# Optimization experiments

Measured on AMD Instinct MI355X. Metric: run time of the kernel, lower is better.

## Reference

```python
import jax, jax.numpy as jnp
import numpy as np

EMB = 768
N_HEADS = 12
HEAD_DIM = EMB // N_HEADS
EPS = 1e-5


def _gelu_tanh(x):
    c = jnp.sqrt(jnp.asarray(2.0 / jnp.pi, x.dtype))
    return 0.5 * x * (1.0 + jnp.tanh(c * (x + 0.044715 * x ** 3)))


def _layernorm(x, scale, shift):
    mean = jnp.mean(x, axis=-1, keepdims=True)
    var = jnp.mean((x - mean) ** 2, axis=-1, keepdims=True)
    return (x - mean) / jnp.sqrt(var + EPS) * scale + shift


def setup_inputs() -> dict:
    key = jax.random.key(0)
    ks = jax.random.split(key, 8)
    s = 0.02  # GPT-2 style init scale
    x = jax.random.normal(ks[0], (8, 1024, EMB), dtype=jnp.float32)
    # torch Linear weights are (out, in); no biases (qkv_bias=False everywhere)
    wq = jax.random.normal(ks[1], (EMB, EMB), dtype=jnp.float32) * s
    wk = jax.random.normal(ks[2], (EMB, EMB), dtype=jnp.float32) * s
    wv = jax.random.normal(ks[3], (EMB, EMB), dtype=jnp.float32) * s
    wo = jax.random.normal(ks[4], (EMB, EMB), dtype=jnp.float32) * s
    w1 = jax.random.normal(ks[5], (4 * EMB, EMB), dtype=jnp.float32) * s
    w2 = jax.random.normal(ks[6], (EMB, 4 * EMB), dtype=jnp.float32) * s
    ln1_scale = jnp.ones((EMB,), jnp.float32)
    ln1_shift = jnp.zeros((EMB,), jnp.float32)
    ln2_scale = jnp.ones((EMB,), jnp.float32)
    ln2_shift = jnp.zeros((EMB,), jnp.float32)
    return dict(x=x, wq=wq, wk=wk, wv=wv, wo=wo, w1=w1, w2=w2,
                ln1_scale=ln1_scale, ln1_shift=ln1_shift,
                ln2_scale=ln2_scale, ln2_shift=ln2_shift)


def reference(x, wq, wk, wv, wo, w1, w2, ln1_scale, ln1_shift, ln2_scale, ln2_shift):
    B, T, E = x.shape
    # --- attention sublayer (pre-LN) ---
    h = _layernorm(x, ln1_scale, ln1_shift)
    q = (h @ wq.T).reshape(B, T, N_HEADS, HEAD_DIM).transpose(0, 2, 1, 3)
    k = (h @ wk.T).reshape(B, T, N_HEADS, HEAD_DIM).transpose(0, 2, 1, 3)
    v = (h @ wv.T).reshape(B, T, N_HEADS, HEAD_DIM).transpose(0, 2, 1, 3)
    scores = jnp.einsum('bhqd,bhkd->bhqk', q, k)  # [B,H,T,T]
    causal = jnp.tril(jnp.ones((T, T), dtype=bool))
    scores = jnp.where(causal, scores, -jnp.inf)
    attn = jax.nn.softmax(scores / np.sqrt(HEAD_DIM), axis=-1)
    ctx = jnp.einsum('bhqk,bhkd->bhqd', attn, v)
    ctx = ctx.transpose(0, 2, 1, 3).reshape(B, T, E)
    x = x + ctx @ wo.T
    # --- FFN sublayer (pre-LN) ---
    h = _layernorm(x, ln2_scale, ln2_shift)
    h = _gelu_tanh(h @ w1.T) @ w2.T
    return x + h
```

## Files before the change

### kernel.cpp

```cpp
#include <hip/hip_runtime.h>
#include <hip/hip_bf16.h>
#include <cstdint>

#define EMB    768
#define NHEADS 12
#define HDIM   64
#define SEQ    1024
#define BATCH  8
#define MROWS  (BATCH*SEQ)
#define FFN    3072
#define W2E    (EMB*EMB)
#define W4E    (FFN*EMB)

typedef __bf16 bf16_t;
typedef bf16_t bf16x8 __attribute__((ext_vector_type(8)));
typedef float  f32x4  __attribute__((ext_vector_type(4)));

__device__ __forceinline__ float b2f(unsigned short u) {
    union { unsigned int i; float f; } t; t.i = ((unsigned int)u) << 16; return t.f;
}
__device__ __forceinline__ unsigned short f2b(float f) {
    union { float f; unsigned int i; } t; t.f = f;
    unsigned int lsb = (t.i >> 16) & 1u;
    t.i += 0x7fffu + lsb;
    return (unsigned short)(t.i >> 16);
}
__device__ __forceinline__ float fexp2(float x) {
#if defined(__has_builtin)
#if __has_builtin(__builtin_amdgcn_exp2f)
    return __builtin_amdgcn_exp2f(x);
#else
    return exp2f(x);
#endif
#else
    return exp2f(x);
#endif
}
__device__ __forceinline__ float frcp(float x) {
#if defined(__has_builtin)
#if __has_builtin(__builtin_amdgcn_rcpf)
    return __builtin_amdgcn_rcpf(x);
#else
    return 1.f / x;
#endif
#else
    return 1.f / x;
#endif
}
__device__ __forceinline__ float gelu_f(float x) {
    float x2 = x * x;
    float u  = x * __builtin_fmaf(x2, -0.10294823f, -2.3022082f);
    return x * frcp(1.f + fexp2(u));
}

#if defined(__has_builtin)
#if __has_builtin(__builtin_amdgcn_global_load_lds)
#define HAS_GLL 1
#endif
#endif
#ifndef HAS_GLL
#define HAS_GLL 0
#endif

__device__ __forceinline__ void gll16(const unsigned short* g, unsigned short* lds_wave_base) {
#if HAS_GLL
    __builtin_amdgcn_global_load_lds(
        (const __attribute__((address_space(1))) unsigned int*)g,
        (__attribute__((address_space(3))) unsigned int*)lds_wave_base, 16, 0, 0);
#endif
}
__device__ __forceinline__ void stage16(const unsigned short* g, unsigned short* lds_wave_base, int lane) {
#if HAS_GLL
    __builtin_amdgcn_global_load_lds(
        (const __attribute__((address_space(1))) unsigned int*)g,
        (__attribute__((address_space(3))) unsigned int*)lds_wave_base, 16, 0, 0);
#else
    *reinterpret_cast<int4*>(lds_wave_base + lane * 8) = *reinterpret_cast<const int4*>(g);
#endif
}

__device__ __forceinline__ int4 load8(const void* src, size_t eoff, bool f32) {
    if (f32) {
        const float4* p = reinterpret_cast<const float4*>((const float*)src + eoff);
        float4 a = p[0], b = p[1];
        union { unsigned short u[8]; int4 v; } r;
        r.u[0] = f2b(a.x); r.u[1] = f2b(a.y); r.u[2] = f2b(a.z); r.u[3] = f2b(a.w);
        r.u[4] = f2b(b.x); r.u[5] = f2b(b.y); r.u[6] = f2b(b.z); r.u[7] = f2b(b.w);
        return r.v;
    }
    return *reinterpret_cast<const int4*>((const unsigned short*)src + eoff);
}
__device__ __forceinline__ float4 load4f(const void* src, size_t eoff, bool f32) {
    if (f32) return *reinterpret_cast<const float4*>((const float*)src + eoff);
    ushort4 u = *reinterpret_cast<const ushort4*>((const unsigned short*)src + eoff);
    float4 r; r.x = b2f(u.x); r.y = b2f(u.y); r.z = b2f(u.z); r.w = b2f(u.w);
    return r;
}

struct DetectArgs { const unsigned short* p[11]; int n[11]; };

__global__ __launch_bounds__(256) void detect_all(DetectArgs a, int* __restrict__ flags) {
    __shared__ int cnt;
    if (threadIdx.x == 0) cnt = 0;
    __syncthreads();
    const unsigned short* src = a.p[blockIdx.x];
    int npairs = a.n[blockIdx.x] / 2;
    if (npairs > 4096) npairs = 4096;
    int local = 0;
    for (int p = threadIdx.x; p < npairs; p += 256) {
        unsigned short u0 = src[2 * p], u1 = src[2 * p + 1];
        int e0 = (u0 >> 7) & 0xFF;
        bool insane0 = (e0 == 0xFF) || (u0 != 0 && (e0 < 96 || e0 > 159));
        bool zpat    = (u0 == 0 && u1 != 0);
        if (insane0 || zpat) ++local;
    }
    atomicAdd(&cnt, local);
    __syncthreads();
    if (threadIdx.x == 0) flags[blockIdx.x] = (cnt * 8 > npairs) ? 1 : 0;
}

__global__ __launch_bounds__(256) void cvt_adapt(
        const void* __restrict__ src, unsigned short* __restrict__ dst,
        int n, const int* __restrict__ flag) {
    int i = blockIdx.x * 256 + threadIdx.x;
    if (i * 4 >= n) return;
    if (*flag) {
        float4 f = reinterpret_cast<const float4*>(src)[i];
        ushort4 o;
        o.x = f2b(f.x); o.y = f2b(f.y); o.z = f2b(f.z); o.w = f2b(f.w);
        reinterpret_cast<ushort4*>(dst)[i] = o;
    } else {
        reinterpret_cast<ushort4*>(dst)[i] = reinterpret_cast<const ushort4*>(src)[i];
    }
}

struct CvtArgs {
    const void* src[6];
    unsigned short* dst[6];
    int n[6];
    int blkoff[7];
    const int* F;
    int fidx[6];
};
__global__ __launch_bounds__(256) void cvt_weights(CvtArgs a) {
    int b = blockIdx.x, seg = 0;
    #pragma unroll
    for (int s = 0; s < 6; ++s) if (b >= a.blkoff[s + 1]) seg = s + 1;
    int i = (b - a.blkoff[seg]) * 256 + threadIdx.x;
    if (i * 4 >= a.n[seg]) return;
    if (a.F[a.fidx[seg]]) {
        float4 f = reinterpret_cast<const float4*>(a.src[seg])[i];
        ushort4 o;
        o.x = f2b(f.x); o.y = f2b(f.y); o.z = f2b(f.z); o.w = f2b(f.w);
        reinterpret_cast<ushort4*>(a.dst[seg])[i] = o;
    } else {
        reinterpret_cast<ushort4*>(a.dst[seg])[i] =
            reinterpret_cast<const ushort4*>(a.src[seg])[i];
    }
}

__global__ __launch_bounds__(256) void reduce2_kernel(
        const float* __restrict__ P, const unsigned short* __restrict__ resid,
        float* __restrict__ out, int n4) {
    int i = blockIdx.x * 256 + threadIdx.x;
    if (i >= n4) return;
    float4 a = reinterpret_cast<const float4*>(P)[i];
    float4 b = reinterpret_cast<const float4*>(P + (size_t)MROWS * EMB)[i];
    ushort4 r = reinterpret_cast<const ushort4*>(resid)[i];
    float4 o;
    o.x = a.x + b.x + b2f(r.x);
    o.y = a.y + b.y + b2f(r.y);
    o.z = a.z + b.z + b2f(r.z);
    o.w = a.w + b.w + b2f(r.w);
    reinterpret_cast<float4*>(out)[i] = o;
}

__global__ __launch_bounds__(256) void ln_kernel(
        const void* __restrict__ x,     const int* __restrict__ fx,
        const void* __restrict__ scale, const int* __restrict__ fsc,
        const void* __restrict__ shift, const int* __restrict__ fsh,
        unsigned short* __restrict__ out) {
    const bool xf = fx && *fx, scf = fsc && *fsc, shf = fsh && *fsh;
    int wave = threadIdx.x >> 6;
    int lane = threadIdx.x & 63;
    int row  = blockIdx.x * 4 + wave;
    const size_t rbase = (size_t)row * EMB;
    float v[12];
    float s = 0.f, s2 = 0.f;
    #pragma unroll
    for (int i = 0; i < 3; ++i) {
        float4 a = load4f(x, rbase + i * 256 + lane * 4, xf);
        v[i*4+0] = a.x; v[i*4+1] = a.y; v[i*4+2] = a.z; v[i*4+3] = a.w;
        s  += a.x + a.y + a.z + a.w;
        s2 += a.x*a.x + a.y*a.y + a.z*a.z + a.w*a.w;
    }
    #pragma unroll
    for (int off = 1; off < 64; off <<= 1) {
        s  += __shfl_xor(s,  off);
        s2 += __shfl_xor(s2, off);
    }
    float mean = s * (1.f / EMB);
    float var  = fmaxf(s2 * (1.f / EMB) - mean * mean, 0.f);
    float rstd = rsqrtf(var + 1e-5f);
    unsigned short* orow = out + rbase;
    #pragma unroll
    for (int i = 0; i < 3; ++i) {
        float4 sc = load4f(scale, i * 256 + lane * 4, scf);
        float4 sh = load4f(shift, i * 256 + lane * 4, shf);
        ushort4 o;
        o.x = f2b((v[i*4+0] - mean) * rstd * sc.x + sh.x);
        o.y = f2b((v[i*4+1] - mean) * rstd * sc.y + sh.y);
        o.z = f2b((v[i*4+2] - mean) * rstd * sc.z + sh.z);
        o.w = f2b((v[i*4+3] - mean) * rstd * sc.w + sh.w);
        *reinterpret_cast<ushort4*>(orow + i * 256 + lane * 4) = o;
    }
}

template<bool GELU, bool RESID, bool OUTF32>
__global__ __launch_bounds__(256, 3) void gemm_lds(
        const unsigned short* __restrict__ A,
        const unsigned short* __restrict__ W,
        const void* R, const int* __restrict__ fR, size_t rOff,
        void* C, int M, int N, int K, int lda, int ldw) {
    constexpr int BK = 32;
    __shared__ __align__(16) unsigned short sA[2][128 * BK];
    __shared__ __align__(16) unsigned short sB[2][128 * BK];
    const int m0 = blockIdx.x * 128, n0 = blockIdx.y * 128;
    const int kz = blockIdx.z;
    const int t = threadIdx.x, wave = t >> 6;
    const int lane = t & 63;
    const int wrow = (wave >> 1) * 64, wcol = (wave & 1) * 64;
    const int quad = lane >> 4, lr = lane & 15;
    const int r0 = t >> 2;
    const int scg = (t & 3) ^ ((t >> 3) & 3);
    const int c0 = scg * 8;
    const int xq = quad ^ ((lr >> 1) & 3);
    const bool rf = fR && *fR;

    A += (size_t)kz * K;
    W += (size_t)kz * K;

    f32x4 acc[4][4];
    #pragma unroll
    for (int i = 0; i < 4; ++i)
        #pragma unroll
        for (int j = 0; j < 4; ++j)
            acc[i][j] = (f32x4){0.f, 0.f, 0.f, 0.f};

    const unsigned short* gA0 = A + (size_t)(m0 + r0) * lda + c0;
    const unsigned short* gA1 = A + (size_t)(m0 + 64 + r0) * lda + c0;
    const unsigned short* gB0 = W + (size_t)(n0 + r0) * ldw + c0;
    const unsigned short* gB1 = W + (size_t)(n0 + 64 + r0) * ldw + c0;

#if HAS_GLL
    gll16(gA0, sA[0] + wave * 512);
    gll16(gA1, sA[0] + 2048 + wave * 512);
    gll16(gB0, sB[0] + wave * 512);
    gll16(gB1, sB[0] + 2048 + wave * 512);
#else
    *reinterpret_cast<int4*>(sA[0] + t * 8)        = *reinterpret_cast<const int4*>(gA0);
    *reinterpret_cast<int4*>(sA[0] + 2048 + t * 8) = *reinterpret_cast<const int4*>(gA1);
    *reinterpret_cast<int4*>(sB[0] + t * 8)        = *reinterpret_cast<const int4*>(gB0);
    *reinterpret_cast<int4*>(sB[0] + 2048 + t * 8) = *reinterpret_cast<const int4*>(gB1);
#endif
    __syncthreads();

    int buf = 0;
    for (int k0 = 0; k0 < K; k0 += BK) {
        if (k0 + BK < K) {
            const int pf = buf ^ 1;
            const int kn = k0 + BK;
#if HAS_GLL
            gll16(gA0 + kn, sA[pf] + wave * 512);
            gll16(gA1 + kn, sA[pf] + 2048 + wave * 512);
            gll16(gB0 + kn, sB[pf] + wave * 512);
            gll16(gB1 + kn, sB[pf] + 2048 + wave * 512);
#else
            *reinterpret_cast<int4*>(sA[pf] + t * 8)        = *reinterpret_cast<const int4*>(gA0 + kn);
            *reinterpret_cast<int4*>(sA[pf] + 2048 + t * 8) = *reinterpret_cast<const int4*>(gA1 + kn);
            *reinterpret_cast<int4*>(sB[pf] + t * 8)        = *reinterpret_cast<const int4*>(gB0 + kn);
            *reinterpret_cast<int4*>(sB[pf] + 2048 + t * 8) = *reinterpret_cast<const int4*>(gB1 + kn);
#endif
        }
        bf16x8 af[4], bfv[4];
        #pragma unroll
        for (int i = 0; i < 4; ++i)
            af[i] = *reinterpret_cast<const bf16x8*>(
                sA[buf] + (wrow >> 6) * 2048 + (i * 16 + lr) * 32 + xq * 8);
        #pragma unroll
        for (int j = 0; j < 4; ++j)
            bfv[j] = *reinterpret_cast<const bf16x8*>(
                sB[buf] + (wcol >> 6) * 2048 + (j * 16 + lr) * 32 + xq * 8);
        #pragma unroll
        for (int i = 0; i < 4; ++i)
            #pragma unroll
            for (int j = 0; j < 4; ++j)
                acc[i][j] = __builtin_amdgcn_mfma_f32_16x16x32_bf16(af[i], bfv[j], acc[i][j], 0, 0, 0);
        __syncthreads();
        buf ^= 1;
    }

    float* Cf = (float*)C + (size_t)kz * M * N;
    #pragma unroll
    for (int i = 0; i < 4; ++i) {
        #pragma unroll
        for (int j = 0; j < 4; ++j) {
            #pragma unroll
            for (int r = 0; r < 4; ++r) {
                int row = m0 + wrow + i * 16 + quad * 4 + r;
                int col = n0 + wcol + j * 16 + lr;
                float val = acc[i][j][r];
                if (GELU) val = gelu_f(val);
                size_t idx = (size_t)row * N + col;
                if (RESID) {
                    float rv = rf ? ((const float*)R)[idx + rOff]
                                  : b2f(((const unsigned short*)R)[idx + rOff]);
                    val += rv;
                }
                if (OUTF32) Cf[idx] = val;
                else {
                    bf16_t hv = (bf16_t)val;
                    ((unsigned short*)C)[idx] = *reinterpret_cast<unsigned short*>(&hv);
                }
            }
        }
    }
}

template<bool GELU, bool RESID, bool OUTF32>
__global__ __launch_bounds__(256) void gemm_bt(
        const unsigned short* __restrict__ A,
        const void* __restrict__ W, const int* __restrict__ fW,
        const void* R, const int* __restrict__ fR, size_t rOff,
        void* C,
        int M, int N, int K) {
    const bool wf = fW && *fW;
    const bool rf = fR && *fR;
    constexpr int BK = 32, PAD = 8, LDW = BK + PAD;
    __shared__ __align__(16) unsigned short sA[128 * LDW];
    __shared__ __align__(16) unsigned short sB[128 * LDW];
    const int m0 = blockIdx.x * 128;
    const int n0 = blockIdx.y * 128;
    const int t    = threadIdx.x;
    const int wave = t >> 6, lane = t & 63;
    const int wrow = (wave >> 1) * 64, wcol = (wave & 1) * 64;
    const int quad = lane >> 4, lr = lane & 15;
    const int srow = t >> 2, scol = (t & 3) * 8;

    f32x4 acc[4][4];
    #pragma unroll
    for (int i = 0; i < 4; ++i)
        #pragma unroll
        for (int j = 0; j < 4; ++j)
            acc[i][j] = (f32x4){0.f, 0.f, 0.f, 0.f};

    const size_t aBase = (size_t)(m0 + srow) * K + scol;
    const size_t bBase = (size_t)(n0 + srow) * K + scol;

    for (int k0 = 0; k0 < K; k0 += BK) {
        int4 av0 = *reinterpret_cast<const int4*>(A + aBase + k0);
        int4 av1 = *reinterpret_cast<const int4*>(A + aBase + (size_t)64 * K + k0);
        int4 bv0 = load8(W, bBase + k0, wf);
        int4 bv1 = load8(W, bBase + (size_t)64 * K + k0, wf);
        *reinterpret_cast<int4*>(sA + srow * LDW + scol)        = av0;
        *reinterpret_cast<int4*>(sA + (srow + 64) * LDW + scol) = av1;
        *reinterpret_cast<int4*>(sB + srow * LDW + scol)        = bv0;
        *reinterpret_cast<int4*>(sB + (srow + 64) * LDW + scol) = bv1;
        __syncthreads();
        bf16x8 af[4], bfv[4];
        #pragma unroll
        for (int i = 0; i < 4; ++i)
            af[i] = *reinterpret_cast<const bf16x8*>(sA + (wrow + i * 16 + lr) * LDW + quad * 8);
        #pragma unroll
        for (int j = 0; j < 4; ++j)
            bfv[j] = *reinterpret_cast<const bf16x8*>(sB + (wcol + j * 16 + lr) * LDW + quad * 8);
        #pragma unroll
        for (int i = 0; i < 4; ++i)
            #pragma unroll
            for (int j = 0; j < 4; ++j)
                acc[i][j] = __builtin_amdgcn_mfma_f32_16x16x32_bf16(af[i], bfv[j], acc[i][j], 0, 0, 0);
        __syncthreads();
    }

    #pragma unroll
    for (int i = 0; i < 4; ++i) {
        #pragma unroll
        for (int j = 0; j < 4; ++j) {
            #pragma unroll
            for (int r = 0; r < 4; ++r) {
                int row = m0 + wrow + i * 16 + quad * 4 + r;
                int col = n0 + wcol + j * 16 + lr;
                float val = acc[i][j][r];
                if (GELU) val = gelu_f(val);
                size_t idx = (size_t)row * N + col;
                if (RESID) {
                    float rv = rf ? ((const float*)R)[idx + rOff]
                                  : b2f(((const unsigned short*)R)[idx + rOff]);
                    val += rv;
                }
                if (OUTF32) ((float*)C)[idx] = val;
                else        ((unsigned short*)C)[idx] = f2b(val);
            }
        }
    }
}

__global__ __launch_bounds__(256) void fattn_kernel(
        const unsigned short* __restrict__ q,
        const unsigned short* __restrict__ k,
        const unsigned short* __restrict__ v,
        int rs, unsigned short* __restrict__ ctx) {
    constexpr int VTP = 72;
    __shared__ __align__(16) unsigned short sK[2][64 * 64];
    __shared__ __align__(16) unsigned short Vt[2][64 * VTP];
    __shared__ __align__(16) unsigned short Pl[4][16 * VTP];
    const int tid  = threadIdx.x;
    const int wave = tid >> 6, lane = tid & 63;
    const int quad = lane >> 4, lr = lane & 15;
    const int NH   = gridDim.x >> 3;
    const int head = blockIdx.x % NH;
    const int pr   = blockIdx.x / NH;
    const int bb   = head / NHEADS, hd = head % NHEADS;
    const size_t seqbase = (size_t)bb * SEQ;
    constexpr float C2 = 0.18033688011112042f;

    const int krow0 = tid >> 3;
    const int dreal = ((tid & 7) * 8) ^ ((krow0 & 7) << 3);
    const int vrow = tid >> 2;
    const int vcol = (tid & 3) * 16;
    const int vxr  = vrow ^ ((tid & 3) << 4);
    const int kswz = (lr & 7) << 3;
    const int pswr = ((lr >> 2) & 3) << 3;
    unsigned short* Pw = Pl[wave];

    #pragma unroll
    for (int seg = 0; seg < 2; ++seg) {
        const int qt = seg == 0 ? (15 - pr) : pr;
        const int q0 = qt * 64 + wave * 16;

        bf16x8 aQ0, aQ1;
        {
            const unsigned short* qp = q + (seqbase + q0 + lr) * rs + hd * HDIM + quad * 8;
            aQ0 = *reinterpret_cast<const bf16x8*>(qp);
            aQ1 = *reinterpret_cast<const bf16x8*>(qp + 32);
        }

        f32x4 O[4];
        #pragma unroll
        for (int i = 0; i < 4; ++i) O[i] = (f32x4){0.f, 0.f, 0.f, 0.f};
        float mrow[4], lrow[4];
        #pragma unroll
        for (int r = 0; r < 4; ++r) { mrow[r] = -__builtin_inff(); lrow[r] = 0.f; }

        {
            const unsigned short* kp = k + (seqbase + krow0) * rs + hd * HDIM + dreal;
            stage16(kp,                   &sK[0][wave * 512],        lane);
            stage16(kp + (size_t)32 * rs, &sK[0][2048 + wave * 512], lane);
            const unsigned short* vp = v + (seqbase + vrow) * rs + hd * HDIM + vcol;
            union { int4 v4; unsigned short u[8]; } pa, pb;
            pa.v4 = *reinterpret_cast<const int4*>(vp);
            pb.v4 = *reinterpret_cast<const int4*>(vp + 8);
            #pragma unroll
            for (int e = 0; e < 8; ++e) Vt[0][(vcol + e) * VTP + vxr]     = pa.u[e];
            #pragma unroll
            for (int e = 0; e < 8; ++e) Vt[0][(vcol + 8 + e) * VTP + vxr] = pb.u[e];
        }
        __syncthreads();

        for (int kt = 0; kt <= qt; ++kt) {
            const int b = kt & 1;
            union { int4 v4; unsigned short u[8]; } ua, ub;
            if (kt < qt) {
                const unsigned short* kp = k + (seqbase + (size_t)(kt + 1) * 64 + krow0) * rs
                                         + hd * HDIM + dreal;
                stage16(kp,                   &sK[b ^ 1][wave * 512],        lane);
                stage16(kp + (size_t)32 * rs, &sK[b ^ 1][2048 + wave * 512], lane);
                const unsigned short* vp = v + (seqbase + (size_t)(kt + 1) * 64 + vrow) * rs
                                         + hd * HDIM + vcol;
                ua.v4 = *reinterpret_cast<const int4*>(vp);
                ub.v4 = *reinterpret_cast<const int4*>(vp + 8);
            }

            f32x4 S[4];
            #pragma unroll
            for (int sub = 0; sub < 4; ++sub) {
                const unsigned short* kr = &sK[b][(sub * 16 + lr) * 64];
                bf16x8 b0 = *reinterpret_cast<const bf16x8*>(kr + ((quad * 8) ^ kswz));
                bf16x8 b1 = *reinterpret_cast<const bf16x8*>(kr + ((32 + quad * 8) ^ kswz));
                f32x4 accS = (f32x4){0.f, 0.f, 0.f, 0.f};
                accS = __builtin_amdgcn_mfma_f32_16x16x32_bf16(aQ0, b0, accS, 0, 0, 0);
                accS = __builtin_amdgcn_mfma_f32_16x16x32_bf16(aQ1, b1, accS, 0, 0, 0);
                S[sub] = accS;
            }
            const bool diag = (kt == qt);
            #pragma unroll
            for (int sub = 0; sub < 4; ++sub) {
                const int kg = kt * 64 + sub * 16 + lr;
                #pragma unroll
                for (int r = 0; r < 4; ++r) {
                    float s = S[sub][r] * C2;
                    if (diag && kg > q0 + quad * 4 + r) s = -__builtin_inff();
                    S[sub][r] = s;
                }
            }
            float mnew[4], alpha[4];
            #pragma unroll
            for (int r = 0; r < 4; ++r) {
                float mx = fmaxf(fmaxf(S[0][r], S[1][r]), fmaxf(S[2][r], S[3][r]));
                #pragma unroll
                for (int m = 1; m < 16; m <<= 1) mx = fmaxf(mx, __shfl_xor(mx, m));
                mnew[r]  = fmaxf(mrow[r], mx);
                alpha[r] = fexp2(mrow[r] - mnew[r]);
                mrow[r]  = mnew[r];
            }
            float rsum[4] = {0.f, 0.f, 0.f, 0.f};
            #pragma unroll
            for (int sub = 0; sub < 4; ++sub)
                #pragma unroll
                for (int r = 0; r < 4; ++r) {
                    float p = fexp2(S[sub][r] - mnew[r]);
                    S[sub][r] = p;
                    rsum[r] += p;
                }
            #pragma unroll
            for (int r = 0; r < 4; ++r) {
                float rs2 = rsum[r];
                #pragma unroll
                for (int m = 1; m < 16; m <<= 1) rs2 += __shfl_xor(rs2, m);
                lrow[r] = lrow[r] * alpha[r] + rs2;
            }

            #pragma unroll
            for (int sub = 0; sub < 4; ++sub)
                #pragma unroll
                for (int r = 0; r < 4; ++r) {
                    bf16_t hv = (bf16_t)S[sub][r];
                    Pw[(quad * 4 + r) * VTP + ((sub * 16 + lr) ^ (quad << 3))] =
                        *reinterpret_cast<unsigned short*>(&hv);
                }
            if (kt < qt) {
                #pragma unroll
                for (int e = 0; e < 8; ++e) Vt[b ^ 1][(vcol + e) * VTP + vxr]     = ua.u[e];
                #pragma unroll
                for (int e = 0; e < 8; ++e) Vt[b ^ 1][(vcol + 8 + e) * VTP + vxr] = ub.u[e];
            }
            #pragma unroll
            for (int d = 0; d < 4; ++d)
                #pragma unroll
                for (int r = 0; r < 4; ++r)
                    O[d][r] *= alpha[r];

            #pragma unroll
            for (int c = 0; c < 2; ++c) {
                bf16x8 aP = *reinterpret_cast<const bf16x8*>(
                    &Pw[lr * VTP + ((c * 32 + quad * 8) ^ pswr)]);
                #pragma unroll
                for (int d = 0; d < 4; ++d) {
                    bf16x8 bV = *reinterpret_cast<const bf16x8*>(
                        &Vt[b][(d * 16 + lr) * VTP + ((c * 32 + quad * 8) ^ (d << 4))]);
                    O[d] = __builtin_amdgcn_mfma_f32_16x16x32_bf16(aP, bV, O[d], 0, 0, 0);
                }
            }
            __syncthreads();
        }

        #pragma unroll
        for (int r = 0; r < 4; ++r) {
            const float rinv = 1.f / lrow[r];
            const int qg = q0 + quad * 4 + r;
            unsigned short* crow = ctx + (seqbase + qg) * EMB + hd * HDIM;
            #pragma unroll
            for (int d = 0; d < 4; ++d)
                crow[d * 16 + lr] = f2b(O[d][r] * rinv);
        }
    }
}

extern "C" void kernel_launch(void* const* d_in, const int* in_sizes, int n_in,
                              void* d_out, int out_size, void* d_ws, size_t ws_size,
                              hipStream_t stream) {
    const void* x  = d_in[0];
    const void* wq = d_in[1], *wk = d_in[2], *wv = d_in[3], *wo = d_in[4];
    const void* w1 = d_in[5], *w2 = d_in[6];
    const void* g1 = d_in[7], *s1 = d_in[8], *g2 = d_in[9], *s2 = d_in[10];
    char* ws = (char*)d_ws;
    dim3 blk(256);

    int* F = (int*)ws;
    {
        DetectArgs da;
        for (int i = 0; i < 11; ++i) { da.p[i] = (const unsigned short*)d_in[i]; da.n[i] = in_sizes[i]; }
        detect_all<<<11, blk, 0, stream>>>(da, F);
    }

    const size_t SZE = (size_t)MROWS * EMB;
    const size_t SZB = SZE * 2;
    unsigned short* base = (unsigned short*)(ws + 256);
    dim3 g768(MROWS / 128, EMB / 128);

    const size_t FULLB = 256 + 2ULL * (2 * W4E) + 2ULL * (4 * W2E)
                       + 2ULL * ((size_t)MROWS * 2304) + 2 * SZB
                       + 2ULL * ((size_t)MROWS * FFN);
    const size_t FULLB2 = FULLB + 2ULL * SZE * 4;

    if (ws_size >= FULLB2) {
        unsigned short* w1b   = base;
        unsigned short* w2b   = w1b + W4E;
        unsigned short* wqkvb = w2b + W4E;
        unsigned short* wob   = wqkvb + 3 * W2E;
        unsigned short* P     = wob + W2E;
        unsigned short* B0    = P + (size_t)MROWS * 2304;
        unsigned short* B1    = B0 + SZE;
        unsigned short* G     = B1 + SZE;
        float*          PK    = (float*)(G + (size_t)MROWS * FFN);

        {
            CvtArgs ca;
            ca.src[0] = wq; ca.src[1] = wk; ca.src[2] = wv;
            ca.src[3] = wo; ca.src[4] = w1; ca.src[5] = w2;
            ca.dst[0] = wqkvb; ca.dst[1] = wqkvb + W2E; ca.dst[2] = wqkvb + 2 * W2E;
            ca.dst[3] = wob;   ca.dst[4] = w1b;         ca.dst[5] = w2b;
            ca.n[0] = ca.n[1] = ca.n[2] = ca.n[3] = W2E; ca.n[4] = ca.n[5] = W4E;
            int off = 0;
            for (int s = 0; s < 6; ++s) { ca.blkoff[s] = off; off += ca.n[s] / 1024; }
            ca.blkoff[6] = off;
            ca.F = F;
            ca.fidx[0] = 1; ca.fidx[1] = 2; ca.fidx[2] = 3;
            ca.fidx[3] = 4; ca.fidx[4] = 5; ca.fidx[5] = 6;
            cvt_weights<<<off, blk, 0, stream>>>(ca);
        }

        ln_kernel<<<MROWS / 4, blk, 0, stream>>>(x, F+0, g1, F+7, s1, F+8, B1);
        dim3 gqkv(MROWS / 128, 2304 / 128);
        gemm_lds<false, false, false><<<gqkv, blk, 0, stream>>>(B1, wqkvb, nullptr, nullptr, 0, P, MROWS, 2304, EMB, EMB, EMB);
        fattn_kernel<<<BATCH * NHEADS * 8, blk, 0, stream>>>(P, P + 768, P + 1536, 2304, B0);
        gemm_lds<false, true, false><<<g768, blk, 0, stream>>>(B0, wob, x, F+0, 0, B1, MROWS, EMB, EMB, EMB, EMB);
        ln_kernel<<<MROWS / 4, blk, 0, stream>>>(B1, nullptr, g2, F+9, s2, F+10, B0);
        dim3 gffn1(MROWS / 128, FFN / 128);
        gemm_lds<true, false, false><<<gffn1, blk, 0, stream>>>(B0, w1b, nullptr, nullptr, 0, G, MROWS, FFN, EMB, EMB, EMB);
        dim3 gsk(MROWS / 128, EMB / 128, 2);
        gemm_lds<false, false, true><<<gsk, blk, 0, stream>>>(G, w2b, nullptr, nullptr, 0, PK, MROWS, EMB, FFN / 2, FFN, FFN);
        reduce2_kernel<<<(SZE / 4 + 255) / 256, blk, 0, stream>>>(PK, B1, (float*)d_out, SZE / 4);
    } else if (ws_size >= FULLB) {
        unsigned short* w1b   = base;
        unsigned short* w2b   = w1b + W4E;
        unsigned short* wqkvb = w2b + W4E;
        unsigned short* wob   = wqkvb + 3 * W2E;
        unsigned short* P     = wob + W2E;
        unsigned short* B0    = P + (size_t)MROWS * 2304;
        unsigned short* B1    = B0 + SZE;
        unsigned short* G     = B1 + SZE;

        {
            CvtArgs ca;
            ca.src[0] = wq; ca.src[1] = wk; ca.src[2] = wv;
            ca.src[3] = wo; ca.src[4] = w1; ca.src[5] = w2;
            ca.dst[0] = wqkvb; ca.dst[1] = wqkvb + W2E; ca.dst[2] = wqkvb + 2 * W2E;
            ca.dst[3] = wob;   ca.dst[4] = w1b;         ca.dst[5] = w2b;
            ca.n[0] = ca.n[1] = ca.n[2] = ca.n[3] = W2E; ca.n[4] = ca.n[5] = W4E;
            int off = 0;
            for (int s = 0; s < 6; ++s) { ca.blkoff[s] = off; off += ca.n[s] / 1024; }
            ca.blkoff[6] = off;
            ca.F = F;
            ca.fidx[0] = 1; ca.fidx[1] = 2; ca.fidx[2] = 3;
            ca.fidx[3] = 4; ca.fidx[4] = 5; ca.fidx[5] = 6;
            cvt_weights<<<off, blk, 0, stream>>>(ca);
        }

        ln_kernel<<<MROWS / 4, blk, 0, stream>>>(x, F+0, g1, F+7, s1, F+8, B1);
        dim3 gqkv(MROWS / 128, 2304 / 128);
        gemm_lds<false, false, false><<<gqkv, blk, 0, stream>>>(B1, wqkvb, nullptr, nullptr, 0, P, MROWS, 2304, EMB, EMB, EMB);
        fattn_kernel<<<BATCH * NHEADS * 8, blk, 0, stream>>>(P, P + 768, P + 1536, 2304, B0);
        gemm_lds<false, true, false><<<g768, blk, 0, stream>>>(B0, wob, x, F+0, 0, B1, MROWS, EMB, EMB, EMB, EMB);
        ln_kernel<<<MROWS / 4, blk, 0, stream>>>(B1, nullptr, g2, F+9, s2, F+10, B0);
        dim3 gffn1(MROWS / 128, FFN / 128);
        gemm_lds<true, false, false><<<gffn1, blk, 0, stream>>>(B0, w1b, nullptr, nullptr, 0, G, MROWS, FFN, EMB, EMB, EMB);
        gemm_lds<false, true, true><<<g768, blk, 0, stream>>>(G, w2b, B1, nullptr, 0, d_out, MROWS, EMB, FFN, FFN, FFN);
    } else if (ws_size >= 256 + 4 * SZB) {
        unsigned short* B0 = base;
        unsigned short* B1 = B0 + SZE;
        unsigned short* B2 = B1 + SZE;
        unsigned short* B3 = B2 + SZE;
        ln_kernel<<<MROWS / 4, blk, 0, stream>>>(x, F+0, g1, F+7, s1, F+8, B0);
        gemm_bt<false, false, false><<<g768, blk, 0, stream>>>(B0, wq, F+1, nullptr, nullptr, 0, B1, MROWS, EMB, EMB);
        gemm_bt<false, false, false><<<g768, blk, 0, stream>>>(B0, wk, F+2, nullptr, nullptr, 0, B2, MROWS, EMB, EMB);
        gemm_bt<false, false, false><<<g768, blk, 0, stream>>>(B0, wv, F+3, nullptr, nullptr, 0, B3, MROWS, EMB, EMB);
        fattn_kernel<<<BATCH * NHEADS * 8, blk, 0, stream>>>(B1, B2, B3, EMB, B0);
        gemm_bt<false, true, false><<<g768, blk, 0, stream>>>(B0, wo, F+4, x, F+0, 0, B1, MROWS, EMB, EMB);
        ln_kernel<<<MROWS / 4, blk, 0, stream>>>(B1, nullptr, g2, F+9, s2, F+10, B2);
        dim3 c3072(2048 / 128, FFN / 128), c768(2048 / 128, EMB / 128);
        for (int c = 0; c < 4; ++c) {
            const size_t r0 = (size_t)c * 2048;
            gemm_bt<true, false, false><<<c3072, blk, 0, stream>>>(B2 + r0 * EMB, w1, F+5, nullptr, nullptr, 0, B3, 2048, FFN, EMB);
            gemm_bt<false, true, true><<<c768, blk, 0, stream>>>(B3, w2, F+6, B1 + r0 * EMB, nullptr, 0, (float*)d_out + r0 * EMB, 2048, EMB, FFN);
        }
    } else {
        unsigned short* hlow = (unsigned short*)d_out;
        unsigned short* x2up = (unsigned short*)d_out + SZE;
        unsigned short* wsQ = base;
        unsigned short* wsK = wsQ + (size_t)1024 * EMB;
        unsigned short* wsV = wsK + (size_t)1024 * EMB;
        unsigned short* wsC = wsV + (size_t)1024 * EMB;
        ln_kernel<<<MROWS / 4, blk, 0, stream>>>(x, F+0, g1, F+7, s1, F+8, hlow);
        dim3 q768(1024 / 128, EMB / 128);
        for (int grp = 0; grp < BATCH; ++grp) {
            const size_t r0 = (size_t)grp * 1024;
            gemm_bt<false, false, false><<<q768, blk, 0, stream>>>(hlow + r0 * EMB, wq, F+1, nullptr, nullptr, 0, wsQ, 1024, EMB, EMB);
            gemm_bt<false, false, false><<<q768, blk, 0, stream>>>(hlow + r0 * EMB, wk, F+2, nullptr, nullptr, 0, wsK, 1024, EMB, EMB);
            gemm_bt<false, false, false><<<q768, blk, 0, stream>>>(hlow + r0 * EMB, wv, F+3, nullptr, nullptr, 0, wsV, 1024, EMB, EMB);
            fattn_kernel<<<1 * NHEADS * 8, blk, 0, stream>>>(wsQ, wsK, wsV, EMB, wsC);
            gemm_bt<false, true, false><<<q768, blk, 0, stream>>>(wsC, wo, F+4, x, F+0, r0 * EMB, x2up + r0 * EMB, 1024, EMB, EMB);
        }
        unsigned short* xb = base;
        unsigned short* h2 = xb + (size_t)1024 * EMB;
        unsigned short* gb = h2 + (size_t)1024 * EMB;
        dim3 f3072(1024 / 128, FFN / 128), f768(1024 / 128, EMB / 128);
        for (int c = 0; c < BATCH; ++c) {
            const size_t r0 = (size_t)c * 1024;
            hipMemcpyAsync(xb, x2up + r0 * EMB, (size_t)1024 * EMB * 2,
                           hipMemcpyDeviceToDevice, stream);
            ln_kernel<<<1024 / 4, blk, 0, stream>>>(xb, nullptr, g2, F+9, s2, F+10, h2);
            gemm_bt<true, false, false><<<f3072, blk, 0, stream>>>(h2, w1, F+5, nullptr, nullptr, 0, gb, 1024, FFN, EMB);
            gemm_bt<false, true, true><<<f768, blk, 0, stream>>>(gb, w2, F+6, xb, nullptr, 0, (float*)d_out + r0 * EMB, 1024, EMB, FFN);
        }
    }
}
```

Baseline: 390.6 us.

## Triple-buffer GEMM LDS tiles with explicit vmcnt waits and raw barriers

Moves the bf16 GEMM main loop from double-buffered to triple-buffered LDS staging on the global-load-to-LDS path, so prefetches run two K-tiles ahead. It uses explicit s_waitcnt vmcnt counts and a raw s_barrier instead of __syncthreads, so the wait only covers the tile about to be consumed. This aims to hide global load latency better. LDS use per block rises from 32KB to 48KB, which may lower occupancy below the 3 blocks/CU launch bound, and the hand-written waitcnt logic is fragile.

Result: faster. 379.1 us (-2.9%).

```diff
diff --git a/kernel.cpp b/kernel.cpp
--- a/kernel.cpp
+++ b/kernel.cpp
@@ -223,8 +223,8 @@
         const void* R, const int* __restrict__ fR, size_t rOff,
         void* C, int M, int N, int K, int lda, int ldw) {
     constexpr int BK = 32;
-    __shared__ __align__(16) unsigned short sA[2][128 * BK];
-    __shared__ __align__(16) unsigned short sB[2][128 * BK];
+    __shared__ __align__(16) unsigned short sA[3][128 * BK];
+    __shared__ __align__(16) unsigned short sB[3][128 * BK];
     const int m0 = blockIdx.x * 128, n0 = blockIdx.y * 128;
     const int kz = blockIdx.z;
     const int t = threadIdx.x, wave = t >> 6;
@@ -252,53 +252,96 @@
     const unsigned short* gB0 = W + (size_t)(n0 + r0) * ldw + c0;
     const unsigned short* gB1 = W + (size_t)(n0 + 64 + r0) * ldw + c0;
 
+    const int nk = K / BK;
+
 #if HAS_GLL
-    gll16(gA0, sA[0] + wave * 512);
-    gll16(gA1, sA[0] + 2048 + wave * 512);
-    gll16(gB0, sB[0] + wave * 512);
-    gll16(gB1, sB[0] + 2048 + wave * 512);
+    #define STAGE_T(tile, bsel)                                       \
+        do {                                                          \
+            const int kk_ = (tile) * BK;                              \
+            gll16(gA0 + kk_, sA[bsel] + wave * 512);                  \
+            gll16(gA1 + kk_, sA[bsel] + 2048 + wave * 512);           \
+            gll16(gB0 + kk_, sB[bsel] + wave * 512);                  \
+            gll16(gB1 + kk_, sB[bsel] + 2048 + wave * 512);           \
+        } while (0)
+
+    STAGE_T(0, 0);
+    if (nk > 1) {
+        STAGE_T(1, 1);
+        asm volatile("s_waitcnt vmcnt(4)" ::: "memory");
+    } else {
+        asm volatile("s_waitcnt vmcnt(0)" ::: "memory");
+    }
+    __builtin_amdgcn_s_barrier();
+    asm volatile("" ::: "memory");
+
+    int cur = 0;
+    for (int i = 0; i < nk; ++i) {
+        if (i + 2 < nk) {
+            int pf = cur + 2; if (pf >= 3) pf -= 3;
+            STAGE_T(i + 2, pf);
+        }
+        bf16x8 af[4], bfv[4];
+        #pragma unroll
+        for (int ii = 0; ii < 4; ++ii)
+            af[ii] = *reinterpret_cast<const bf16x8*>(
+                sA[cur] + (wrow >> 6) * 2048 + (ii * 16 + lr) * 32 + xq * 8);
+        #pragma unroll
+        for (int j = 0; j < 4; ++j)
+            bfv[j] = *reinterpret_cast<const bf16x8*>(
+                sB[cur] + (wcol >> 6) * 2048 + (j * 16 + lr) * 32 + xq * 8);
+        #pragma unroll
+        for (int ii = 0; ii < 4; ++ii)
+            #pragma unroll
+            for (int j = 0; j < 4; ++j)
+                acc[ii][j] = __builtin_amdgcn_mfma_f32_16x16x32_bf16(af[ii], bfv[j], acc[ii][j], 0, 0, 0);
+        if (i + 2 < nk) {
+            asm volatile("s_waitcnt vmcnt(4)" ::: "memory");
+        } else if (i + 1 < nk) {
+            asm volatile("s_waitcnt vmcnt(0)" ::: "memory");
+        }
+        if (i + 1 < nk) {
+            __builtin_amdgcn_s_barrier();
+            asm volatile("" ::: "memory");
+        }
+        cur += 1; if (cur == 3) cur = 0;
+    }
+    #undef STAGE_T
 #else
-    *reinterpret_cast<int4*>(sA[0] + t * 8)        = *reinterpret_cast<const int4*>(gA0);
-    *reinterpret_cast<int4*>(sA[0] + 2048 + t * 8) = *reinterpret_cast<const int4*>(gA1);
-    *reinterpret_cast<int4*>(sB[0] + t * 8)        = *reinterpret_cast<const int4*>(gB0);
-    *reinterpret_cast<int4*>(sB[0] + 2048 + t * 8) = *reinterpret_cast<const int4*>(gB1);
-#endif
-    __syncthreads();
-
-    int buf = 0;
-    for (int k0 = 0; k0 < K; k0 += BK) {
-        if (k0 + BK < K) {
-            const int pf = buf ^ 1;
-            const int kn = k0 + BK;
-#if HAS_GLL
-            gll16(gA0 + kn, sA[pf] + wave * 512);
-            gll16(gA1 + kn, sA[pf] + 2048 + wave * 512);
-            gll16(gB0 + kn, sB[pf] + wave * 512);
-            gll16(gB1 + kn, sB[pf] + 2048 + wave * 512);
-#else
+    int cur = 0;
+    {
+        *reinterpret_cast<int4*>(sA[0] + t * 8)        = *reinterpret_cast<const int4*>(gA0);
+        *reinterpret_cast<int4*>(sA[0] + 2048 + t * 8) = *reinterpret_cast<const int4*>(gA1);
+        *reinterpret_cast<int4*>(sB[0] + t * 8)        = *reinterpret_cast<const int4*>(gB0);
+        *reinterpret_cast<int4*>(sB[0] + 2048 + t * 8) = *reinterpret_cast<const int4*>(gB1);
+        __syncthreads();
+    }
+    for (int i = 0; i < nk; ++i) {
+        if (i + 1 < nk) {
+            int pf = cur ^ 1;
+            const int kn = (i + 1) * BK;
             *reinterpret_cast<int4*>(sA[pf] + t * 8)        = *reinterpret_cast<const int4*>(gA0 + kn);
             *reinterpret_cast<int4*>(sA[pf] + 2048 + t * 8) = *reinterpret_cast<const int4*>(gA1 + kn);
             *reinterpret_cast<int4*>(sB[pf] + t * 8)        = *reinterpret_cast<const int4*>(gB0 + kn);
             *reinterpret_cast<int4*>(sB[pf] + 2048 + t * 8) = *reinterpret_cast<const int4*>(gB1 + kn);
-#endif
         }
         bf16x8 af[4], bfv[4];
         #pragma unroll
-        for (int i = 0; i < 4; ++i)
-            af[i] = *reinterpret_cast<const bf16x8*>(
-                sA[buf] + (wrow >> 6) * 2048 + (i * 16 + lr) * 32 + xq * 8);
+        for (int ii = 0; ii < 4; ++ii)
+            af[ii] = *reinterpret_cast<const bf16x8*>(
+                sA[cur] + (wrow >> 6) * 2048 + (ii * 16 + lr) * 32 + xq * 8);
         #pragma unroll
         for (int j = 0; j < 4; ++j)
             bfv[j] = *reinterpret_cast<const bf16x8*>(
-                sB[buf] + (wcol >> 6) * 2048 + (j * 16 + lr) * 32 + xq * 8);
-        #pragma unroll
-        for (int i = 0; i < 4; ++i)
+                sB[cur] + (wcol >> 6) * 2048 + (j * 16 + lr) * 32 + xq * 8);
+        #pragma unroll
+        for (int ii = 0; ii < 4; ++ii)
             #pragma unroll
             for (int j = 0; j < 4; ++j)
-                acc[i][j] = __builtin_amdgcn_mfma_f32_16x16x32_bf16(af[i], bfv[j], acc[i][j], 0, 0, 0);
+                acc[ii][j] = __builtin_amdgcn_mfma_f32_16x16x32_bf16(af[ii], bfv[j], acc[ii][j], 0, 0, 0);
         __syncthreads();
-        buf ^= 1;
-    }
+        cur ^= 1;
+    }
+#endif
 
     float* Cf = (float*)C + (size_t)kz * M * N;
     #pragma unroll
```
